# Performance work log

Measured on AMD Instinct MI355X. Metric: run time of the kernel, lower is better.

The kernel has to match this reference:

```python
import jax, jax.numpy as jnp
import numpy as np

HIDDEN = 4096
N_HEADS = 32
N_KV_HEADS = 8
HEAD_DIM = HIDDEN // N_HEADS  # 128
N_GROUPS = N_HEADS // N_KV_HEADS  # 4
MAX_POS = 4096
B, S = 2, 2048


def _rope_tables(max_pos, dim):
    # Mirrors create_sinusoidal_positions: freqs [pos, dim/2] -> emb [pos, dim]
    freqs = np.einsum('i,j->ij', np.arange(max_pos),
                      1.0 / 10000 ** (np.arange(0, dim, 2) / dim)).astype('float32')
    emb = np.concatenate((freqs, freqs), axis=-1)  # [pos, dim]
    return jnp.asarray(np.sin(emb)), jnp.asarray(np.cos(emb))

_SIN, _COS = _rope_tables(MAX_POS, HEAD_DIM)


def _apply_rope(t, sin_pos, cos_pos):
    # t: [B,S,H,hd]; sin/cos: [B,S,1,hd]
    half = t.shape[-1] // 2
    rot = jnp.concatenate((-t[..., half:], t[..., :half]), axis=-1)
    return t * cos_pos + rot * sin_pos


def setup_inputs() -> dict:
    key = jax.random.key(0)
    ks = jax.random.split(key, 5)
    std = 0.02
    hidden_states = jax.random.normal(ks[0], (B, S, HIDDEN), dtype=jnp.float32)
    attention_mask = jnp.ones((B, S), dtype=jnp.float32)
    position_ids = jnp.broadcast_to(jnp.arange(S, dtype=jnp.int32)[None, :], (B, S))
    Wq = jax.random.normal(ks[1], (HIDDEN, N_HEADS * HEAD_DIM), dtype=jnp.float32) * std
    Wk = jax.random.normal(ks[2], (HIDDEN, N_KV_HEADS * HEAD_DIM), dtype=jnp.float32) * std
    Wv = jax.random.normal(ks[3], (HIDDEN, N_KV_HEADS * HEAD_DIM), dtype=jnp.float32) * std
    Wo = jax.random.normal(ks[4], (HIDDEN, HIDDEN), dtype=jnp.float32) * std
    return {'hidden_states': hidden_states, 'attention_mask': attention_mask,
            'position_ids': position_ids, 'Wq': Wq, 'Wk': Wk, 'Wv': Wv, 'Wo': Wo}


def reference(hidden_states, attention_mask, position_ids, Wq, Wk, Wv, Wo):
    b, s, _ = hidden_states.shape
    # QKV projections (no bias) + head split
    q = (hidden_states @ Wq).reshape(b, s, N_HEADS, HEAD_DIM)
    k = (hidden_states @ Wk).reshape(b, s, N_KV_HEADS, HEAD_DIM)
    v = (hidden_states @ Wv).reshape(b, s, N_KV_HEADS, HEAD_DIM)
    # Rotary embedding
    sin_pos = _SIN[position_ids][:, :, None, :]  # [B,S,1,hd]
    cos_pos = _COS[position_ids][:, :, None, :]
    q = _apply_rope(q, sin_pos, cos_pos)
    k = _apply_rope(k, sin_pos, cos_pos)
    # Repeat KV heads for grouped-query attention
    k = jnp.repeat(k, N_GROUPS, axis=2)  # [B,S,H,hd]
    v = jnp.repeat(v, N_GROUPS, axis=2)
    # Causal mask & padding mask -> additive bias
    causal = jnp.tril(jnp.ones((s, s), dtype=bool))[None, None]  # [1,1,S,S]
    pad = (attention_mask > 0)[:, None, None, :]                 # [B,1,1,S]
    mask = jnp.logical_and(causal, pad)
    neg = jnp.finfo(jnp.float32).min
    bias = jnp.where(mask, 0.0, neg).astype(jnp.float32)
    # Scaled dot-product attention (softmax in fp32, matching flax)
    scale = 1.0 / jnp.sqrt(jnp.asarray(HEAD_DIM, dtype=jnp.float32))
    scores = jnp.einsum('bqhd,bkhd->bhqk', q * scale, k) + bias
    attn = jax.nn.softmax(scores, axis=-1)
    out = jnp.einsum('bhqk,bkhd->bqhd', attn, v).reshape(b, s, HIDDEN)
    return out @ Wo
```

## Files before the change

### kernel.cpp

```cpp
#include <hip/hip_runtime.h>

typedef unsigned short u16;
typedef __attribute__((ext_vector_type(8))) short bf16x8;
typedef __attribute__((ext_vector_type(8))) unsigned short u16x8;
typedef __attribute__((ext_vector_type(4))) float f32x4;

#define HIDDEN 4096
#define NH 32
#define NKV 8
#define HD 128
#define BB 2
#define SS 2048
#define TOK (BB * SS)
#define MAXPOS 4096
#define NQKV 6144

__device__ __forceinline__ u16 f2bf(float f) {
  unsigned u = __float_as_uint(f);
  u += 0x7FFFu + ((u >> 16) & 1u);
  return (u16)(u >> 16);
}
__device__ __forceinline__ float bf2f(u16 u) {
  return __uint_as_float(((unsigned)u) << 16);
}

__device__ __forceinline__ void gload_lds16(const u16* g, u16* l) {
  __builtin_amdgcn_global_load_lds(
      (const __attribute__((address_space(1))) unsigned int*)g,
      (__attribute__((address_space(3))) unsigned int*)l, 16, 0, 0);
}

__device__ __forceinline__ u16* swzp(u16* base, int row, int col, int stride) {
  int off = (row * stride + col) * 2;
  off ^= (row & 7) << 4;
  return (u16*)((char*)base + off);
}
__device__ __forceinline__ const u16* swzc(const u16* base, int row, int col, int stride) {
  int off = (row * stride + col) * 2;
  off ^= (row & 7) << 4;
  return (const u16*)((const char*)base + off);
}


__global__ void conv_bf16(const float* __restrict__ X, u16* __restrict__ Y, int n8) {
  int i = blockIdx.x * 256 + threadIdx.x;
  if (i >= n8) return;
  const float4* p = (const float4*)X;
  float4 a = p[2 * (long)i], b = p[2 * (long)i + 1];
  u16x8 o;
  o[0] = f2bf(a.x); o[1] = f2bf(a.y); o[2] = f2bf(a.z); o[3] = f2bf(a.w);
  o[4] = f2bf(b.x); o[5] = f2bf(b.y); o[6] = f2bf(b.z); o[7] = f2bf(b.w);
  *(u16x8*)&Y[(long)i * 8] = o;
}

__global__ __launch_bounds__(256) void conv_transpose(const float* __restrict__ W,
                                                      u16* __restrict__ Wt,
                                                      int K, int N) {
  __shared__ float tile[64][65];
  const int n0 = blockIdx.x * 64, k0 = blockIdx.y * 64;
  const int t = threadIdx.x;
  const int r = t >> 4, c4 = (t & 15) * 4;
#pragma unroll
  for (int i = 0; i < 4; i++) {
    float4 v = *(const float4*)&W[(long)(k0 + r + i * 16) * N + n0 + c4];
    tile[r + i * 16][c4 + 0] = v.x;
    tile[r + i * 16][c4 + 1] = v.y;
    tile[r + i * 16][c4 + 2] = v.z;
    tile[r + i * 16][c4 + 3] = v.w;
  }
  __syncthreads();
#pragma unroll
  for (int i = 0; i < 4; i++) {
    int n = r + i * 16;
    ushort4 o;
    o.x = f2bf(tile[c4 + 0][n]);
    o.y = f2bf(tile[c4 + 1][n]);
    o.z = f2bf(tile[c4 + 2][n]);
    o.w = f2bf(tile[c4 + 3][n]);
    *(ushort4*)&Wt[(long)(n0 + n) * K + k0 + c4] = o;
  }
}


__global__ void rope_table(float* __restrict__ st, float* __restrict__ ct) {
  int i = blockIdx.x * 256 + threadIdx.x;
  int pos = i >> 6, j = i & 63;
  float inv = exp2f(-(float)(2 * j) * (13.287712379549449f / 128.f));
  float a = (float)pos * inv;
  st[i] = sinf(a);
  ct[i] = cosf(a);
}

__global__ void rope_apply(u16* __restrict__ T, const int* __restrict__ pid,
                           const float* __restrict__ st, const float* __restrict__ ct,
                           int nh, int total, float scale) {
  int i = blockIdx.x * 256 + threadIdx.x;
  if (i >= total) return;
  int j = i & 63;
  int rest = i >> 6;
  int h = rest % nh;
  int tok = rest / nh;
  int pos = pid[tok];
  long base = ((long)tok * nh + h) * 128;
  float c = ct[pos * 64 + j], s = st[pos * 64 + j];
  float a = bf2f(T[base + j]), b = bf2f(T[base + 64 + j]);
  T[base + j]      = f2bf((a * c - b * s) * scale);
  T[base + 64 + j] = f2bf((b * c + a * s) * scale);
}

__global__ __launch_bounds__(256) void vtrans(const u16* __restrict__ V, u16* __restrict__ Vt) {
  __shared__ u16 tile[64][68];
  const int s0 = blockIdx.x * 64, d0 = blockIdx.y * 64;
  const int bk = blockIdx.z;
  const int b = bk >> 3, kvh = bk & 7;
  const int t = threadIdx.x;
  const int r = t >> 4, c4 = (t & 15) * 4;
#pragma unroll
  for (int i = 0; i < 4; i++) {
    int s = s0 + r + i * 16;
    ushort4 v = *(const ushort4*)&V[(((long)b * SS + s) * NKV + kvh) * HD + d0 + c4];
    tile[r + i * 16][c4 + 0] = v.x;
    tile[r + i * 16][c4 + 1] = v.y;
    tile[r + i * 16][c4 + 2] = v.z;
    tile[r + i * 16][c4 + 3] = v.w;
  }
  __syncthreads();
#pragma unroll
  for (int i = 0; i < 4; i++) {
    int d = r + i * 16;
    ushort4 o;
    o.x = tile[c4 + 0][d];
    o.y = tile[c4 + 1][d];
    o.z = tile[c4 + 2][d];
    o.w = tile[c4 + 3][d];
    *(ushort4*)&Vt[(((long)bk) * HD + d0 + d) * SS + s0 + c4] = o;
  }
}


#define GEMM256_CORE(Aptr, Btptr, Kd)                                              \
  __shared__ __align__(16) u16 ring[65536];       \
  const int tid = threadIdx.x;                                                     \
  const int lane = tid & 63;                                                       \
  const int wid = tid >> 6;                                                        \
  const int wm = wid >> 2, wn = wid & 3;                                           \
  const int fr = lane & 15, fq = lane >> 4;                                        \
  const int sr = tid >> 2;                                 \
  const int ss = (tid & 3) ^ ((sr ^ (sr >> 2)) & 3);        \
  const int csl = (fq ^ ((fr ^ (fr >> 2)) & 3)) << 4;      \
  const u16* Ag0 = (Aptr) + (brow + sr) * (long)(Kd) + ss * 8;                     \
  const u16* Bg0 = (Btptr) + (bcol + sr) * (long)(Kd) + ss * 8;                    \
  f32x4 acc[8][4] = {};                                                            \
  auto stage = [&](int tt) {                                                       \
    u16* as_ = &ring[(tt & 3) * 16384];                                            \
    const u16* ag = Ag0 + (long)tt * 32;                                           \
    const u16* bg = Bg0 + (long)tt * 32;                                           \
    gload_lds16(ag, as_ + tid * 8);                                                \
    gload_lds16(ag + 128 * (long)(Kd), as_ + 4096 + tid * 8);                      \
    gload_lds16(bg, as_ + 8192 + tid * 8);                                         \
    gload_lds16(bg + 128 * (long)(Kd), as_ + 12288 + tid * 8);                     \
  };                                                                               \
  const int NT = (Kd) / 32;                                                        \
  stage(0); stage(1); stage(2);                                                    \
  _Pragma("unroll 1")                                                              \
  for (int t = 0; t < NT; ++t) {                                                   \
    if (t + 2 < NT)      asm volatile("s_waitcnt vmcnt(8)" ::: "memory");          \
    else if (t + 1 < NT) asm volatile("s_waitcnt vmcnt(4)" ::: "memory");          \
    else                 asm volatile("s_waitcnt vmcnt(0)" ::: "memory");          \
    __builtin_amdgcn_s_barrier();                                                  \
    __builtin_amdgcn_sched_barrier(0);                                             \
    if (t + 3 < NT) stage(t + 3);      \
    const u16* as_ = &ring[(t & 3) * 16384];                                       \
    bf16x8 af[8], bfv[4];                                                          \
    _Pragma("unroll") for (int m = 0; m < 8; m++)                                  \
      af[m] = *(const bf16x8*)((const char*)as_ +                                  \
                               ((wm * 128 + m * 16 + fr) << 6) + csl);             \
    _Pragma("unroll") for (int n = 0; n < 4; n++)                                  \
      bfv[n] = *(const bf16x8*)((const char*)as_ + 16384 +                         \
                                ((wn * 64 + n * 16 + fr) << 6) + csl);             \
    asm volatile("s_waitcnt lgkmcnt(0)" ::: "memory");                             \
    __builtin_amdgcn_sched_barrier(0);                                             \
    __builtin_amdgcn_s_setprio(1);                                                 \
    _Pragma("unroll") for (int m = 0; m < 8; m++)                                  \
      _Pragma("unroll") for (int n = 0; n < 4; n++)                                \
        acc[m][n] = __builtin_amdgcn_mfma_f32_16x16x32_bf16(af[m], bfv[n],         \
                                                            acc[m][n], 0, 0, 0);   \
    __builtin_amdgcn_s_setprio(0);                                                 \
  }

#define XCD_BLOCK_MAP()                                                            \
  const int nwg = gridDim.x * gridDim.y;                                           \
  int bid = blockIdx.y * gridDim.x + blockIdx.x;                                   \
  bid = (bid & 7) * (nwg >> 3) + (bid >> 3);                                       \
  const long brow = (long)(bid / gridDim.x) * 256;                                 \
  const long bcol = (long)(bid % gridDim.x) * 256;

__global__ __launch_bounds__(512) void gemm_qkv(const u16* __restrict__ A,
                                                const u16* __restrict__ Bt,
                                                u16* __restrict__ Qb,
                                                u16* __restrict__ Kb,
                                                u16* __restrict__ Vb) {
  XCD_BLOCK_MAP()
  GEMM256_CORE(A, Bt, HIDDEN)
  u16* dst;
  long nst, cb;
  if (bcol < 4096)      { dst = Qb; nst = 4096; cb = bcol; }
  else if (bcol < 5120) { dst = Kb; nst = 1024; cb = bcol - 4096; }
  else                  { dst = Vb; nst = 1024; cb = bcol - 5120; }
#pragma unroll
  for (int m = 0; m < 8; m++)
#pragma unroll
    for (int j = 0; j < 4; j++) {
      long row = brow + wm * 128 + m * 16 + fq * 4 + j;
#pragma unroll
      for (int n = 0; n < 4; n++)
        dst[row * nst + cb + wn * 64 + n * 16 + fr] = f2bf(acc[m][n][j]);
    }
}

__global__ __launch_bounds__(512) void gemm_out(const u16* __restrict__ A,
                                                const u16* __restrict__ Bt,
                                                float* __restrict__ C) {
  XCD_BLOCK_MAP()
  GEMM256_CORE(A, Bt, HIDDEN)
#pragma unroll
  for (int m = 0; m < 8; m++)
#pragma unroll
    for (int j = 0; j < 4; j++) {
      long row = brow + wm * 128 + m * 16 + fq * 4 + j;
#pragma unroll
      for (int n = 0; n < 4; n++)
        C[row * HIDDEN + bcol + wn * 64 + n * 16 + fr] = acc[m][n][j];
    }
}


__global__ __launch_bounds__(256) void attn_fwd(const u16* __restrict__ Q,
                                                const u16* __restrict__ K,
                                                const u16* __restrict__ Vt,
                                                const float* __restrict__ amask,
                                                u16* __restrict__ O) {
  const int b = blockIdx.z, h = blockIdx.y;
  const int qi = gridDim.x - 1 - blockIdx.x;
  const int qb = qi * 64;
  const int kvh = h >> 2;
  const int t = threadIdx.x, lane = t & 63, w = t >> 6;
  const int fr = lane & 15, fq = lane >> 4;

  __shared__ u16 KlA[64 * 128];
  __shared__ u16 VlA[128 * 64];
  __shared__ u16 PlA[4][16 * 64];

  bf16x8 qf[4];
  {
    const int qrow = qb + w * 16 + fr;
    const long qbase = (((long)b * SS + qrow) * NH + h) * HD;
#pragma unroll
    for (int kk = 0; kk < 4; kk++)
      qf[kk] = *(const bf16x8*)&Q[qbase + kk * 32 + fq * 8];
  }

  const u16* Kh = K + (long)b * SS * NKV * HD + (long)kvh * HD;
  const u16* Vh = Vt + ((long)b * NKV + kvh) * (long)HD * SS;
  const float* Mh = amask + (long)b * SS;
  u16* Plw = PlA[w];

  const int kst = t >> 4, kcol = (t & 15) * 8;
  const int vst = t >> 3, vcol = (t & 7) * 8;

  bf16x8 kreg[4], vreg[4];
  auto load_tile = [&](int kv0) {
#pragma unroll
    for (int i = 0; i < 4; i++)
      kreg[i] = *(const bf16x8*)&Kh[(long)(kv0 + kst + i * 16) * (NKV * HD) + kcol];
#pragma unroll
    for (int i = 0; i < 4; i++)
      vreg[i] = *(const bf16x8*)&Vh[(long)(vst + i * 32) * SS + kv0 + vcol];
  };
  auto write_tile = [&]() {
#pragma unroll
    for (int i = 0; i < 4; i++)
      *(bf16x8*)swzp(KlA, kst + i * 16, kcol, 128) = kreg[i];
#pragma unroll
    for (int i = 0; i < 4; i++)
      *(bf16x8*)swzp(VlA, vst + i * 32, vcol, 64) = vreg[i];
  };

  f32x4 oacc[8] = {};
  float mrow[4], lrow[4];
#pragma unroll
  for (int j = 0; j < 4; j++) { mrow[j] = -1e30f; lrow[j] = 0.f; }
  int qr0 = qb + w * 16 + fq * 4;
  const float L2E = 1.4426950408889634f;

  const int ntiles = qi + 1;
  load_tile(0);
  write_tile();
  __syncthreads();
  if (ntiles > 1) load_tile(64);

  for (int kvt = 0; kvt < ntiles; kvt++) {
    const int kv0 = kvt * 64;

    float mk[4];
#pragma unroll
    for (int n = 0; n < 4; n++) mk[n] = Mh[kv0 + n * 16 + fr];

    f32x4 sacc[4] = {};
#pragma unroll
    for (int n = 0; n < 4; n++)
#pragma unroll
      for (int kk = 0; kk < 4; kk++) {
        bf16x8 kf = *(const bf16x8*)swzc(KlA, n * 16 + fr, kk * 32 + fq * 8, 128);
        sacc[n] = __builtin_amdgcn_mfma_f32_16x16x32_bf16(qf[kk], kf, sacc[n], 0, 0, 0);
      }

    const bool diag = (kvt == qi);
#pragma unroll
    for (int n = 0; n < 4; n++) {
      const int key = kv0 + n * 16 + fr;
#pragma unroll
      for (int j = 0; j < 4; j++) {
        float v = sacc[n][j];
        if ((diag && key > qr0 + j) || mk[n] <= 0.f) v = -1e30f;
        sacc[n][j] = v;
      }
    }

    float pm[4];
    bool need = false;
#pragma unroll
    for (int j = 0; j < 4; j++) {
      float mx = fmaxf(fmaxf(sacc[0][j], sacc[1][j]), fmaxf(sacc[2][j], sacc[3][j]));
#pragma unroll
      for (int d = 1; d < 16; d <<= 1) mx = fmaxf(mx, __shfl_xor(mx, d, 64));
      pm[j] = mx;
      need = need || (mx > mrow[j] + 8.f);
    }
    if (__any(need)) {
#pragma unroll
      for (int j = 0; j < 4; j++) {
        float mnew = fmaxf(mrow[j], pm[j]);
        float alpha = exp2f((mrow[j] - mnew) * L2E);
        lrow[j] *= alpha;
        mrow[j] = mnew;
#pragma unroll
        for (int no = 0; no < 8; no++) oacc[no][j] *= alpha;
      }
    }
#pragma unroll
    for (int j = 0; j < 4; j++) {
      float sum = 0.f;
#pragma unroll
      for (int n = 0; n < 4; n++) {
        float pv = exp2f((sacc[n][j] - mrow[j]) * L2E);
        sacc[n][j] = pv;
        sum += pv;
      }
#pragma unroll
      for (int d = 1; d < 16; d <<= 1) sum += __shfl_xor(sum, d, 64);
      lrow[j] += sum;
    }

#pragma unroll
    for (int n = 0; n < 4; n++)
#pragma unroll
      for (int j = 0; j < 4; j++)
        *swzp(Plw, fq * 4 + j, n * 16 + fr, 64) = f2bf(sacc[n][j]);

#pragma unroll
    for (int kk = 0; kk < 2; kk++) {
      bf16x8 pf = *(const bf16x8*)swzc(Plw, fr, kk * 32 + fq * 8, 64);
#pragma unroll
      for (int no = 0; no < 8; no++) {
        bf16x8 vf = *(const bf16x8*)swzc(VlA, no * 16 + fr, kk * 32 + fq * 8, 64);
        oacc[no] = __builtin_amdgcn_mfma_f32_16x16x32_bf16(pf, vf, oacc[no], 0, 0, 0);
      }
    }

    __syncthreads();
    if (kvt + 1 < ntiles) {
      write_tile();
      if (kvt + 2 < ntiles) load_tile((kvt + 2) * 64);
      __syncthreads();
    }
  }

#pragma unroll
  for (int j = 0; j < 4; j++) {
    const int row = qb + w * 16 + fq * 4 + j;
    const float inv = 1.0f / lrow[j];
    const long obase = (((long)b * SS + row) * NH + h) * HD;
#pragma unroll
    for (int no = 0; no < 8; no++)
      O[obase + no * 16 + fr] = f2bf(oacc[no][j] * inv);
  }
}


extern "C" void kernel_launch(void* const* d_in, const int* in_sizes, int n_in,
                              void* d_out, int out_size, void* d_ws, size_t ws_size,
                              hipStream_t stream) {
  const float* hs    = (const float*)d_in[0];
  const float* amask = (const float*)d_in[1];
  const int*   pid   = (const int*)d_in[2];
  const float* Wq    = (const float*)d_in[3];
  const float* Wk    = (const float*)d_in[4];
  const float* Wv    = (const float*)d_in[5];
  const float* Wo    = (const float*)d_in[6];
  float* out = (float*)d_out;

  char* ws = (char*)d_ws;
  const size_t MB = 1024ull * 1024ull;
  u16* Xb    = (u16*)(ws + 0);
  u16* Wqkvt = (u16*)(ws + 32 * MB);
  u16* Wot   = (u16*)(ws + 80 * MB);
  u16* Qb    = (u16*)(ws + 112 * MB);
  u16* Kb    = (u16*)(ws + 144 * MB);
  u16* Vb    = (u16*)(ws + 152 * MB);
  u16* Vtb   = (u16*)(ws + 160 * MB);
  float* st  = (float*)(ws + 168 * MB);
  float* ct  = (float*)(ws + 169 * MB);
  u16* Ab = Xb;

  rope_table<<<(MAXPOS * 64) / 256, 256, 0, stream>>>(st, ct);
  conv_bf16<<<(TOK * HIDDEN / 8) / 256, 256, 0, stream>>>(hs, Xb, TOK * HIDDEN / 8);
  conv_transpose<<<dim3(HIDDEN / 64, HIDDEN / 64), 256, 0, stream>>>(Wq, Wqkvt, HIDDEN, HIDDEN);
  conv_transpose<<<dim3(1024 / 64, HIDDEN / 64), 256, 0, stream>>>(Wk, Wqkvt + 4096ull * 4096, HIDDEN, 1024);
  conv_transpose<<<dim3(1024 / 64, HIDDEN / 64), 256, 0, stream>>>(Wv, Wqkvt + 5120ull * 4096, HIDDEN, 1024);
  conv_transpose<<<dim3(HIDDEN / 64, HIDDEN / 64), 256, 0, stream>>>(Wo, Wot, HIDDEN, HIDDEN);

  gemm_qkv<<<dim3(NQKV / 256, TOK / 256), 512, 0, stream>>>(Xb, Wqkvt, Qb, Kb, Vb);

  const float qscale = 0.08838834764831845f;
  rope_apply<<<(TOK * NH * 64) / 256, 256, 0, stream>>>(Qb, pid, st, ct, NH, TOK * NH * 64, qscale);
  rope_apply<<<(TOK * NKV * 64) / 256, 256, 0, stream>>>(Kb, pid, st, ct, NKV, TOK * NKV * 64, 1.0f);

  vtrans<<<dim3(SS / 64, HD / 64, BB * NKV), 256, 0, stream>>>(Vb, Vtb);

  attn_fwd<<<dim3(SS / 64, NH, BB), 256, 0, stream>>>(Qb, Kb, Vtb, amask, Ab);

  gemm_out<<<dim3(HIDDEN / 256, TOK / 256), 512, 0, stream>>>(Ab, Wot, out);
}
```

Before: 817.3 us.

## Double-buffer attention K/V tiles via direct global-to-LDS loads, transpose S layout

The attention kernel now double-buffers K and V tiles in LDS and fills them with direct global-to-LDS loads (gload_lds16) using precomputed swizzled offsets, replacing the register staging and write-back step. QK^T is computed transposed so each lane owns one query row, which simplifies the max and sum reductions to two cross-lane shuffles. A per-tile padding flag computed by a small new kernel lets the loop skip mask loads for fully unmasked tiles, and s_setprio hints raise priority around the MFMA blocks. LDS usage roughly doubles, which may reduce occupancy.

```diff
diff --git a/kernel.cpp b/kernel.cpp
--- a/kernel.cpp
+++ b/kernel.cpp
@@ -106,6 +106,15 @@
   float a = bf2f(T[base + j]), b = bf2f(T[base + 64 + j]);
   T[base + j]      = f2bf((a * c - b * s) * scale);
   T[base + 64 + j] = f2bf((b * c + a * s) * scale);
+}
+
+__global__ void mask_flags(const float* __restrict__ amask, int* __restrict__ mf) {
+  int i = threadIdx.x;
+  if (i >= BB * (SS / 64)) return;
+  int b = i / (SS / 64), tt = i % (SS / 64);
+  int any = 0;
+  for (int k = 0; k < 64; k++) any |= (amask[b * SS + tt * 64 + k] <= 0.f) ? 1 : 0;
+  mf[i] = any;
 }
 
 __global__ __launch_bounds__(256) void vtrans(const u16* __restrict__ V, u16* __restrict__ Vt) {
@@ -239,6 +248,7 @@
                                                 const u16* __restrict__ K,
                                                 const u16* __restrict__ Vt,
                                                 const float* __restrict__ amask,
+                                                const int* __restrict__ mflag,
                                                 u16* __restrict__ O) {
   const int b = blockIdx.z, h = blockIdx.y;
   const int qi = gridDim.x - 1 - blockIdx.x;
@@ -247,13 +257,13 @@
   const int t = threadIdx.x, lane = t & 63, w = t >> 6;
   const int fr = lane & 15, fq = lane >> 4;
 
-  __shared__ u16 KlA[64 * 128];
-  __shared__ u16 VlA[128 * 64];
+  __shared__ u16 Kl[2][64 * 128];
+  __shared__ u16 Vl[2][128 * 64];
   __shared__ u16 PlA[4][16 * 64];
 
+  const int qrow = qb + w * 16 + fr;
   bf16x8 qf[4];
   {
-    const int qrow = qb + w * 16 + fr;
     const long qbase = (((long)b * SS + qrow) * NH + h) * HD;
 #pragma unroll
     for (int kk = 0; kk < 4; kk++)
@@ -263,133 +273,141 @@
   const u16* Kh = K + (long)b * SS * NKV * HD + (long)kvh * HD;
   const u16* Vh = Vt + ((long)b * NKV + kvh) * (long)HD * SS;
   const float* Mh = amask + (long)b * SS;
+  const int* Mf = mflag + b * (SS / 64);
   u16* Plw = PlA[w];
 
-  const int kst = t >> 4, kcol = (t & 15) * 8;
-  const int vst = t >> 3, vcol = (t & 7) * 8;
-
-  bf16x8 kreg[4], vreg[4];
-  auto load_tile = [&](int kv0) {
+  int koff[4], voff[4];
+#pragma unroll
+  for (int i = 0; i < 4; i++) {
+    int o = i * 4096 + t * 16;
+    int rk = o >> 8;
+    int ck = (o & 255) ^ ((rk & 7) << 4);
+    koff[i] = rk * (NKV * HD) + (ck >> 1);
+    int rv = o >> 7;
+    int cv = (o & 127) ^ ((rv & 7) << 4);
+    voff[i] = rv * SS + (cv >> 1);
+  }
+  auto stage = [&](int kv0, int buf) {
+    const u16* Kt = Kh + (long)kv0 * (NKV * HD);
+    const u16* Vs = Vh + kv0;
 #pragma unroll
     for (int i = 0; i < 4; i++)
-      kreg[i] = *(const bf16x8*)&Kh[(long)(kv0 + kst + i * 16) * (NKV * HD) + kcol];
+      gload_lds16(Kt + koff[i], &Kl[buf][i * 2048 + t * 8]);
 #pragma unroll
     for (int i = 0; i < 4; i++)
-      vreg[i] = *(const bf16x8*)&Vh[(long)(vst + i * 32) * SS + kv0 + vcol];
+      gload_lds16(Vs + voff[i], &Vl[buf][i * 2048 + t * 8]);
   };
-  auto write_tile = [&]() {
-#pragma unroll
-    for (int i = 0; i < 4; i++)
-      *(bf16x8*)swzp(KlA, kst + i * 16, kcol, 128) = kreg[i];
-#pragma unroll
-    for (int i = 0; i < 4; i++)
-      *(bf16x8*)swzp(VlA, vst + i * 32, vcol, 64) = vreg[i];
-  };
 
   f32x4 oacc[8] = {};
-  float mrow[4], lrow[4];
-#pragma unroll
-  for (int j = 0; j < 4; j++) { mrow[j] = -1e30f; lrow[j] = 0.f; }
-  int qr0 = qb + w * 16 + fq * 4;
+  float mrow = -1e30f, lrow = 0.f;
   const float L2E = 1.4426950408889634f;
-
-  const int ntiles = qi + 1;
-  load_tile(0);
-  write_tile();
-  __syncthreads();
-  if (ntiles > 1) load_tile(64);
-
-  for (int kvt = 0; kvt < ntiles; kvt++) {
+  const int nt = qi + 1;
+
+  stage(0, 0);
+
+  for (int kvt = 0; kvt < nt; kvt++) {
+    const int cur = kvt & 1;
     const int kv0 = kvt * 64;
 
-    float mk[4];
-#pragma unroll
-    for (int n = 0; n < 4; n++) mk[n] = Mh[kv0 + n * 16 + fr];
+    __syncthreads();
+    if (kvt + 1 < nt) stage(kv0 + 64, cur ^ 1);
+    __builtin_amdgcn_sched_barrier(0);
 
     f32x4 sacc[4] = {};
+    __builtin_amdgcn_s_setprio(1);
 #pragma unroll
     for (int n = 0; n < 4; n++)
 #pragma unroll
       for (int kk = 0; kk < 4; kk++) {
-        bf16x8 kf = *(const bf16x8*)swzc(KlA, n * 16 + fr, kk * 32 + fq * 8, 128);
-        sacc[n] = __builtin_amdgcn_mfma_f32_16x16x32_bf16(qf[kk], kf, sacc[n], 0, 0, 0);
+        bf16x8 kf = *(const bf16x8*)swzc(&Kl[cur][0], n * 16 + fr, kk * 32 + fq * 8, 128);
+        sacc[n] = __builtin_amdgcn_mfma_f32_16x16x32_bf16(kf, qf[kk], sacc[n], 0, 0, 0);
       }
-
-    const bool diag = (kvt == qi);
+    __builtin_amdgcn_s_setprio(0);
+
+    if (kvt == qi) {
+#pragma unroll
+      for (int n = 0; n < 4; n++)
+#pragma unroll
+        for (int j = 0; j < 4; j++) {
+          const int key = kv0 + n * 16 + fq * 4 + j;
+          if (key > qrow) sacc[n][j] = -1e30f;
+        }
+    }
+    if (Mf[kvt]) {
+#pragma unroll
+      for (int n = 0; n < 4; n++) {
+        float4 mkv = *(const float4*)&Mh[kv0 + n * 16 + fq * 4];
+#pragma unroll
+        for (int j = 0; j < 4; j++)
+          if ((&mkv.x)[j] <= 0.f) sacc[n][j] = -1e30f;
+      }
+    }
+
+    float mn[4];
+#pragma unroll
+    for (int n = 0; n < 4; n++)
+      mn[n] = fmaxf(fmaxf(sacc[n][0], sacc[n][1]), fmaxf(sacc[n][2], sacc[n][3]));
+    float mx = fmaxf(fmaxf(mn[0], mn[1]), fmaxf(mn[2], mn[3]));
+    mx = fmaxf(mx, __shfl_xor(mx, 16, 64));
+    mx = fmaxf(mx, __shfl_xor(mx, 32, 64));
+
+    if (__any(mx > mrow + 8.f)) {
+      float mnew = fmaxf(mrow, mx);
+      float alpha = exp2f((mrow - mnew) * L2E);
+      lrow *= alpha;
+      mrow = mnew;
+      float aj[4];
+#pragma unroll
+      for (int j = 0; j < 4; j++) aj[j] = __shfl(alpha, fq * 4 + j, 64);
+#pragma unroll
+      for (int no = 0; no < 8; no++)
+#pragma unroll
+        for (int j = 0; j < 4; j++) oacc[no][j] *= aj[j];
+    }
+
+    float sn[4];
 #pragma unroll
     for (int n = 0; n < 4; n++) {
-      const int key = kv0 + n * 16 + fr;
-#pragma unroll
-      for (int j = 0; j < 4; j++) {
-        float v = sacc[n][j];
-        if ((diag && key > qr0 + j) || mk[n] <= 0.f) v = -1e30f;
-        sacc[n][j] = v;
-      }
-    }
-
-    float pm[4];
-    bool need = false;
-#pragma unroll
-    for (int j = 0; j < 4; j++) {
-      float mx = fmaxf(fmaxf(sacc[0][j], sacc[1][j]), fmaxf(sacc[2][j], sacc[3][j]));
-#pragma unroll
-      for (int d = 1; d < 16; d <<= 1) mx = fmaxf(mx, __shfl_xor(mx, d, 64));
-      pm[j] = mx;
-      need = need || (mx > mrow[j] + 8.f);
-    }
-    if (__any(need)) {
-#pragma unroll
-      for (int j = 0; j < 4; j++) {
-        float mnew = fmaxf(mrow[j], pm[j]);
-        float alpha = exp2f((mrow[j] - mnew) * L2E);
-        lrow[j] *= alpha;
-        mrow[j] = mnew;
-#pragma unroll
-        for (int no = 0; no < 8; no++) oacc[no][j] *= alpha;
-      }
-    }
-#pragma unroll
-    for (int j = 0; j < 4; j++) {
-      float sum = 0.f;
-#pragma unroll
-      for (int n = 0; n < 4; n++) {
-        float pv = exp2f((sacc[n][j] - mrow[j]) * L2E);
-        sacc[n][j] = pv;
-        sum += pv;
-      }
-#pragma unroll
-      for (int d = 1; d < 16; d <<= 1) sum += __shfl_xor(sum, d, 64);
-      lrow[j] += sum;
-    }
-
-#pragma unroll
-    for (int n = 0; n < 4; n++)
 #pragma unroll
       for (int j = 0; j < 4; j++)
-        *swzp(Plw, fq * 4 + j, n * 16 + fr, 64) = f2bf(sacc[n][j]);
-
+        sacc[n][j] = exp2f((sacc[n][j] - mrow) * L2E);
+      sn[n] = (sacc[n][0] + sacc[n][1]) + (sacc[n][2] + sacc[n][3]);
+    }
+    float sum = (sn[0] + sn[1]) + (sn[2] + sn[3]);
+    sum += __shfl_xor(sum, 16, 64);
+    sum += __shfl_xor(sum, 32, 64);
+    lrow += sum;
+
+#pragma unroll
+    for (int n = 0; n < 4; n++) {
+      ushort4 pw;
+      pw.x = f2bf(sacc[n][0]);
+      pw.y = f2bf(sacc[n][1]);
+      pw.z = f2bf(sacc[n][2]);
+      pw.w = f2bf(sacc[n][3]);
+      *(ushort4*)swzp(Plw, fr, n * 16 + fq * 4, 64) = pw;
+    }
+
+    __builtin_amdgcn_s_setprio(1);
 #pragma unroll
     for (int kk = 0; kk < 2; kk++) {
       bf16x8 pf = *(const bf16x8*)swzc(Plw, fr, kk * 32 + fq * 8, 64);
 #pragma unroll
       for (int no = 0; no < 8; no++) {
-        bf16x8 vf = *(const bf16x8*)swzc(VlA, no * 16 + fr, kk * 32 + fq * 8, 64);
+        bf16x8 vf = *(const bf16x8*)swzc(&Vl[cur][0], no * 16 + fr, kk * 32 + fq * 8, 64);
         oacc[no] = __builtin_amdgcn_mfma_f32_16x16x32_bf16(pf, vf, oacc[no], 0, 0, 0);
       }
     }
-
-    __syncthreads();
-    if (kvt + 1 < ntiles) {
-      write_tile();
-      if (kvt + 2 < ntiles) load_tile((kvt + 2) * 64);
-      __syncthreads();
-    }
-  }
-
+    __builtin_amdgcn_s_setprio(0);
+  }
+
+  float lj[4];
+#pragma unroll
+  for (int j = 0; j < 4; j++) lj[j] = __shfl(lrow, fq * 4 + j, 64);
 #pragma unroll
   for (int j = 0; j < 4; j++) {
     const int row = qb + w * 16 + fq * 4 + j;
-    const float inv = 1.0f / lrow[j];
+    const float inv = 1.0f / lj[j];
     const long obase = (((long)b * SS + row) * NH + h) * HD;
 #pragma unroll
     for (int no = 0; no < 8; no++)
@@ -421,9 +439,11 @@
   u16* Vtb   = (u16*)(ws + 160 * MB);
   float* st  = (float*)(ws + 168 * MB);
   float* ct  = (float*)(ws + 169 * MB);
+  int* mf    = (int*)(ws + 170 * MB);
   u16* Ab = Xb;
 
   rope_table<<<(MAXPOS * 64) / 256, 256, 0, stream>>>(st, ct);
+  mask_flags<<<1, 64, 0, stream>>>(amask, mf);
   conv_bf16<<<(TOK * HIDDEN / 8) / 256, 256, 0, stream>>>(hs, Xb, TOK * HIDDEN / 8);
   conv_transpose<<<dim3(HIDDEN / 64, HIDDEN / 64), 256, 0, stream>>>(Wq, Wqkvt, HIDDEN, HIDDEN);
   conv_transpose<<<dim3(1024 / 64, HIDDEN / 64), 256, 0, stream>>>(Wk, Wqkvt + 4096ull * 4096, HIDDEN, 1024);
@@ -438,7 +458,7 @@
 
   vtrans<<<dim3(SS / 64, HD / 64, BB * NKV), 256, 0, stream>>>(Vb, Vtb);
 
-  attn_fwd<<<dim3(SS / 64, NH, BB), 256, 0, stream>>>(Qb, Kb, Vtb, amask, Ab);
+  attn_fwd<<<dim3(SS / 64, NH, BB), 256, 0, stream>>>(Qb, Kb, Vtb, amask, mf, Ab);
 
   gemm_out<<<dim3(HIDDEN / 256, TOK / 256), 512, 0, stream>>>(Ab, Wot, out);
 }
```

Result: faster. 749.0 us, median of 6 (-8.4%).
